# Performance work log

Measured on AMD Instinct MI355X. Metric: run time of the kernel, lower is better.

Reference implementation:

```python
import jax, jax.numpy as jnp
import numpy as np

D_MODEL, HEADS, D_FF = 768, 12, 3072
D_K = D_MODEL // HEADS
EPS = 1e-6


def _norm(x, alpha, bias):
    # NormalizationLayer: scalar alpha/bias, torch.std is unbiased (ddof=1)
    mean = jnp.mean(x, axis=-1, keepdims=True)
    std = jnp.std(x, axis=-1, ddof=1, keepdims=True)
    return alpha * (x - mean) / (std + EPS) + bias


def setup_inputs() -> dict:
    key = jax.random.key(0)
    ks = jax.random.split(key, 16)
    B, S = 2, 4096
    x = jax.random.normal(ks[0], (B, S, D_MODEL), dtype=jnp.float32)
    mask = jax.random.randint(ks[1], (B, 1, 1, S), 0, 2, dtype=jnp.int32)
    w = lambda k, o, i: (jax.random.normal(k, (o, i), dtype=jnp.float32) * 0.02)
    return {
        "x": x, "mask": mask,
        "wq": w(ks[2], D_MODEL, D_MODEL), "bq": jnp.zeros((D_MODEL,), jnp.float32),
        "wk": w(ks[3], D_MODEL, D_MODEL), "bk": jnp.zeros((D_MODEL,), jnp.float32),
        "wv": w(ks[4], D_MODEL, D_MODEL), "bv": jnp.zeros((D_MODEL,), jnp.float32),
        "wo": w(ks[5], D_MODEL, D_MODEL), "bo": jnp.zeros((D_MODEL,), jnp.float32),
        "w1": w(ks[6], D_FF, D_MODEL), "b1": jnp.zeros((D_FF,), jnp.float32),
        "w2": w(ks[7], D_MODEL, D_FF), "b2": jnp.zeros((D_MODEL,), jnp.float32),
        "alpha1": jnp.ones((1,), jnp.float32), "beta1": jnp.ones((1,), jnp.float32),
        "alpha2": jnp.ones((1,), jnp.float32), "beta2": jnp.ones((1,), jnp.float32),
    }


def reference(x, mask, wq, bq, wk, bk, wv, bv, wo, bo, w1, b1, w2, b2,
              alpha1, beta1, alpha2, beta2):
    B, S, _ = x.shape

    # --- residual connection 0: pre-norm + self-attention ---
    h = _norm(x, alpha1, beta1)
    q = (h @ wq.T + bq).reshape(B, S, HEADS, D_K).transpose(0, 2, 1, 3)  # [B,H,S,dk]
    k = (h @ wk.T + bk).reshape(B, S, HEADS, D_K).transpose(0, 2, 1, 3)
    v = (h @ wv.T + bv).reshape(B, S, HEADS, D_K).transpose(0, 2, 1, 3)
    scores = jnp.einsum('bhqd,bhkd->bhqk', q, k) / jnp.sqrt(jnp.float32(D_K))
    scores = jnp.where(mask == 0, jnp.float32(-1e9), scores)
    attn = jax.nn.softmax(scores, axis=-1)
    ctx = jnp.einsum('bhqk,bhkd->bhqd', attn, v)
    ctx = ctx.transpose(0, 2, 1, 3).reshape(B, S, D_MODEL)
    x = x + (ctx @ wo.T + bo)

    # --- residual connection 1: pre-norm + FFN ---
    h = _norm(x, alpha2, beta2)
    ff = jax.nn.relu(h @ w1.T + b1) @ w2.T + b2
    return x + ff
```

## Files before the change

kernel.cpp:

```cpp
#include <hip/hip_runtime.h>
#include <hip/hip_bf16.h>
#include <math.h>


typedef __hip_bfloat16 bf16;
typedef short short8 __attribute__((ext_vector_type(8)));
typedef short short4v __attribute__((ext_vector_type(4)));
typedef float f32x4 __attribute__((ext_vector_type(4)));

#define MFMA(A, B, C) __builtin_amdgcn_mfma_f32_16x16x32_bf16(A, B, C, 0, 0, 0)

#if __has_builtin(__builtin_amdgcn_exp2f)
#define EXP2(x) __builtin_amdgcn_exp2f(x)
#else
#define EXP2(x) exp2f(x)
#endif

#define PSWAP32(a, b) asm("v_permlane32_swap_b32 %0, %1" : "+v"(a), "+v"(b))
#define PSWAP16(a, b) asm("v_permlane16_swap_b32 %0, %1" : "+v"(a), "+v"(b))

__device__ __forceinline__ unsigned cvt_pk(float lo, float hi) {
  unsigned r;
  asm("v_cvt_pk_bf16_f32 %0, %1, %2" : "=v"(r) : "v"(lo), "v"(hi));
  return r;
}

__device__ __forceinline__ void gl_lds16(const void* g, void* l) {
  __builtin_amdgcn_global_load_lds(
      (__attribute__((address_space(1))) void*)g,
      (__attribute__((address_space(3))) void*)l, 16, 0, 0);
}

__device__ __forceinline__ short f2b(float f) {
  bf16 h = __float2bfloat16(f);
  return *reinterpret_cast<short*>(&h);
}

__global__ __launch_bounds__(256)
void prep_all(const float* __restrict__ wq, const float* __restrict__ wk,
              const float* __restrict__ wv, const float* __restrict__ wo,
              const float* __restrict__ w1, const float* __restrict__ w2,
              const float* __restrict__ bq, const float* __restrict__ bk,
              const float* __restrict__ bv, const int* __restrict__ mask,
              bf16* __restrict__ wqkvb, bf16* __restrict__ wob,
              bf16* __restrict__ w1b, bf16* __restrict__ w2b,
              float* __restrict__ bqkv,
              int* __restrict__ pos_g, int* __restrict__ nch_g,
              bf16* __restrict__ kc, bf16* __restrict__ vtc)
{
  const int t = threadIdx.x;
  if (blockIdx.x < 2) {
    const int b = blockIdx.x;
    const int* mb = mask + b * 4096;
    __shared__ int lsum[256];
    int loc = 0;
    int mv[16];
#pragma unroll
    for (int j = 0; j < 16; j++) { mv[j] = mb[t * 16 + j] ? 1 : 0; loc += mv[j]; }
    lsum[t] = loc;
    __syncthreads();
    for (int off = 1; off < 256; off <<= 1) {
      int v = (t >= off) ? lsum[t - off] : 0;
      __syncthreads();
      lsum[t] += v;
      __syncthreads();
    }
    const int nvalid = lsum[255];
    int base = lsum[t] - loc;
#pragma unroll
    for (int j = 0; j < 16; j++) {
      pos_g[b * 4096 + t * 16 + j] = mv[j] ? base : -1;
      if (mv[j]) base++;
    }
    const int npad = (nvalid + 63) & ~63;
    if (t == 0) { nch_g[b * 2] = npad >> 6; nch_g[b * 2 + 1] = npad - nvalid; }
    const int npv = npad - nvalid;
    if (npv > 0) {
      const int krows = 12 * npv;
      const short8 z = {};
      for (int task = t; task < krows * 8; task += 256) {
        const int rr = task >> 3, cc = task & 7;
        const int hh = rr / npv, r = nvalid + rr % npv;
        *(short8*)&kc[(((long)(b * 12 + hh) * 4096) + r) * 64 + cc * 8] = z;
      }
      const int vrows = 12 * 64;
      for (int task = t; task < vrows * npv; task += 256) {
        const int row = task / npv, j = nvalid + task % npv;
        const int hh = row >> 6, d = row & 63;
        vtc[((long)((b * 12 + hh) * 64 + d)) * 4096 + j] = __float2bfloat16(0.f);
      }
    }
    return;
  }
  const int i = (blockIdx.x - 2) * 256 + t;
  const int W = 147456;
  const int F = 589824;
  const float* src; bf16* dst; int off;
  if (i < W)          { src = wq; dst = wqkvb;           off = i; }
  else if (i < 2*W)   { src = wk; dst = wqkvb + 589824;  off = i - W; }
  else if (i < 3*W)   { src = wv; dst = wqkvb + 1179648; off = i - 2*W; }
  else if (i < 4*W)   { src = wo; dst = wob;             off = i - 3*W; }
  else if (i < 4*W+F) { src = w1; dst = w1b;             off = i - 4*W; }
  else                { src = w2; dst = w2b;             off = i - 4*W - F; }
  float4 v = ((const float4*)src)[off];
  short4v o;
  o.x = f2b(v.x); o.y = f2b(v.y); o.z = f2b(v.z); o.w = f2b(v.w);
  ((short4v*)dst)[off] = o;
  if (i < 2304)
    bqkv[i] = (i < 768) ? bq[i] : (i < 1536 ? bk[i - 768] : bv[i - 1536]);
}

template<typename INT>
__global__ __launch_bounds__(256)
void ln_kernel(const INT* __restrict__ x, bf16* __restrict__ out,
               const float* __restrict__ alpha, const float* __restrict__ beta)
{
  const int row = blockIdx.x;
  const long base = (long)row * 768;
  const int t = threadIdx.x;
  float v[3]; float s = 0.f, ss = 0.f;
#pragma unroll
  for (int i = 0; i < 3; i++) {
    v[i] = (float)x[base + t + i * 256];
    s += v[i]; ss += v[i] * v[i];
  }
#pragma unroll
  for (int off = 32; off > 0; off >>= 1) {
    s  += __shfl_down(s, off);
    ss += __shfl_down(ss, off);
  }
  __shared__ float red[8];
  __shared__ float stats[2];
  const int w = t >> 6;
  if ((t & 63) == 0) { red[w] = s; red[4 + w] = ss; }
  __syncthreads();
  if (t == 0) {
    float S  = red[0] + red[1] + red[2] + red[3];
    float SS = red[4] + red[5] + red[6] + red[7];
    float mean = S * (1.f / 768.f);
    float var = fmaxf((SS - 768.f * mean * mean) * (1.f / 767.f), 0.f);
    stats[0] = mean;
    stats[1] = 1.f / (sqrtf(var) + 1e-6f);
  }
  __syncthreads();
  const float mean = stats[0], rinv = stats[1];
  const float a = alpha[0], b = beta[0];
#pragma unroll
  for (int i = 0; i < 3; i++)
    out[base + t + i * 256] = __float2bfloat16(a * (v[i] - mean) * rinv + b);
}

template<int MODE, int TM, typename RT, typename OUTT>
__global__ __launch_bounds__(256)
void gemm_bt(const bf16* __restrict__ A, const bf16* __restrict__ W,
             const float* __restrict__ bias, const RT* __restrict__ R,
             OUTT* __restrict__ Cout, int M, int N, int K)
{
  constexpr int MI = TM / 32;
  __shared__ __align__(16) bf16 sA[TM * 32];
  __shared__ __align__(16) bf16 sB[128 * 32];
  const int t = threadIdx.x;
  const int w = t >> 6, lane = t & 63;
  const int lr = lane & 15, quad = lane >> 4;
  const int tm = blockIdx.x * TM, tn = blockIdx.y * 128;
  const int wm = (w >> 1) * (MI * 16), wn = (w & 1) * 64;

  const int srow = w * 16 + (lane >> 2);
  const int scol = (lane & 3) * 8;
  const bf16* Ap = A + (long)(tm + srow) * K + scol;
  const bf16* Wp = W + (long)(tn + srow) * K + scol;
  bf16* sAp = &sA[srow * 32 + scol];
  bf16* sBp = &sB[srow * 32 + scol];
  const long half = (long)64 * K;

  f32x4 acc[MI][4] = {};

  for (int kb = 0; kb < K; kb += 32) {
    gl_lds16(Ap + kb, sAp);
    if (TM == 128) gl_lds16(Ap + kb + half, sAp + 64 * 32);
    gl_lds16(Wp + kb, sBp);
    gl_lds16(Wp + kb + half, sBp + 64 * 32);
    __syncthreads();
    short8 af[MI], bfr[4];
#pragma unroll
    for (int i = 0; i < MI; i++)
      af[i] = *(const short8*)&sA[(wm + i * 16 + lr) * 32 + quad * 8];
#pragma unroll
    for (int j = 0; j < 4; j++)
      bfr[j] = *(const short8*)&sB[(wn + j * 16 + lr) * 32 + quad * 8];
#pragma unroll
    for (int i = 0; i < MI; i++)
#pragma unroll
      for (int j = 0; j < 4; j++)
        acc[i][j] = MFMA(af[i], bfr[j], acc[i][j]);
    __syncthreads();
  }

#pragma unroll
  for (int i = 0; i < MI; i++) {
#pragma unroll
    for (int j = 0; j < 4; j++) {
      const int col = tn + wn + j * 16 + lr;
      const float bv = bias[col];
#pragma unroll
      for (int r = 0; r < 4; r++) {
        const int m = tm + wm + i * 16 + quad * 4 + r;
        float vv = acc[i][j][r] + bv;
        if (MODE == 1) vv = fmaxf(vv, 0.f);
        if (MODE == 4) vv += (float)R[(long)m * N + col];
        Cout[(long)m * N + col] = (OUTT)vv;
      }
    }
  }
}

__global__ __launch_bounds__(256)
void gemm_qkv(const bf16* __restrict__ A, const bf16* __restrict__ W,
              const float* __restrict__ bias, const int* __restrict__ pos_g,
              bf16* __restrict__ Qo, bf16* __restrict__ Kc, bf16* __restrict__ Vtc)
{
  const int K = 768;
  __shared__ __align__(16) bf16 sA[128 * 32];
  __shared__ __align__(16) bf16 sB[128 * 32];
  const int t = threadIdx.x;
  const int w = t >> 6, lane = t & 63;
  const int lr = lane & 15, quad = lane >> 4;
  const int tm = blockIdx.x * 128, tn = blockIdx.y * 128;
  const int wm = (w >> 1) * 64, wn = (w & 1) * 64;

  const int srow = w * 16 + (lane >> 2);
  const int scol = (lane & 3) * 8;
  const bf16* Ap = A + (long)(tm + srow) * K + scol;
  const bf16* Wp = W + (long)(tn + srow) * K + scol;
  bf16* sAp = &sA[srow * 32 + scol];
  bf16* sBp = &sB[srow * 32 + scol];
  const long half = (long)64 * K;

  f32x4 acc[4][4] = {};

  for (int kb = 0; kb < K; kb += 32) {
    gl_lds16(Ap + kb, sAp);
    gl_lds16(Ap + kb + half, sAp + 64 * 32);
    gl_lds16(Wp + kb, sBp);
    gl_lds16(Wp + kb + half, sBp + 64 * 32);
    __syncthreads();
    short8 af[4], bfr[4];
#pragma unroll
    for (int i = 0; i < 4; i++)
      af[i] = *(const short8*)&sA[(wm + i * 16 + lr) * 32 + quad * 8];
#pragma unroll
    for (int j = 0; j < 4; j++)
      bfr[j] = *(const short8*)&sB[(wn + j * 16 + lr) * 32 + quad * 8];
#pragma unroll
    for (int i = 0; i < 4; i++)
#pragma unroll
      for (int j = 0; j < 4; j++)
        acc[i][j] = MFMA(af[i], bfr[j], acc[i][j]);
    __syncthreads();
  }

  const int region = (tn >= 1536) ? 2 : (tn >= 768 ? 1 : 0);
#pragma unroll
  for (int i = 0; i < 4; i++) {
#pragma unroll
    for (int j = 0; j < 4; j++) {
      const int col = tn + wn + j * 16 + lr;
      const int c768 = col - region * 768;
      const int hh = c768 >> 6, d = c768 & 63;
      const float bv = bias[col];
#pragma unroll
      for (int r = 0; r < 4; r++) {
        const int m = tm + wm + i * 16 + quad * 4 + r;
        const int bb = m >> 12, sdx = m & 4095;
        float vv = acc[i][j][r] + bv;
        if (region == 0) {
          vv *= 0.18033688011112042f;
          Qo[((long)(bb * 12 + hh) * 4096 + sdx) * 64 + d] = __float2bfloat16(vv);
        } else {
          const int p_ = pos_g[bb * 4096 + sdx];
          if (p_ >= 0) {
            if (region == 1)
              Kc[((long)(bb * 12 + hh) * 4096 + p_) * 64 + d] = __float2bfloat16(vv);
            else
              Vtc[((long)(bb * 12 + hh) * 64 + d) * 4096 + p_] = __float2bfloat16(vv);
          }
        }
      }
    }
  }
}

__global__ __launch_bounds__(256)
void attn_kernel(const bf16* __restrict__ Q, const bf16* __restrict__ Kg,
                 const bf16* __restrict__ Vt,
                 const int* __restrict__ nch_g, bf16* __restrict__ ctx)
{
  __shared__ __align__(16) bf16 sK[2][64 * 64];
  __shared__ __align__(16) bf16 sV[2][64 * 64];

  const int t = threadIdx.x, w = t >> 6, lane = t & 63;
  const int lr = lane & 15, quad = lane >> 4;
  const int bh = blockIdx.y, b = bh / 12, hh = bh % 12;
  const int qb = blockIdx.x * 128 + w * 32;
  const long bh_s = (long)bh * 4096;
  const int nch = nch_g[b * 2];
  const int npv = nch_g[b * 2 + 1];

  short8 qf[2][2];
#pragma unroll
  for (int qt = 0; qt < 2; qt++) {
    const bf16* qp = Q + (bh_s + qb + qt * 16 + lr) * 64 + quad * 8;
    qf[qt][0] = *(const short8*)qp;
    qf[qt][1] = *(const short8*)(qp + 32);
  }

  const int rA = w * 16 + (lane >> 3), rB = rA + 8;
  const int c8 = lane & 7;
  const bf16* kA = Kg + (bh_s + rA) * 64 + ((c8 ^ (rA & 7)) << 3);
  const bf16* kB = Kg + (bh_s + rB) * 64 + ((c8 ^ (rB & 7)) << 3);
  const bf16* vA = Vt + ((long)bh * 64 + rA) * 4096 + ((c8 ^ (rA & 7)) << 3);
  const bf16* vB = Vt + ((long)bh * 64 + rB) * 4096 + ((c8 ^ (rB & 7)) << 3);
  const int ldsA = (w * 16) * 64 + lane * 8;
  const int ldsB = ldsA + 8 * 64;

  const int cA = (quad * 8) ^ ((lr & 7) << 3);

  float l_part[2] = {};
  f32x4 Ot[4][2] = {};

  auto stage = [&](int kc, int buf) {
    gl_lds16(kA + (long)kc * 64, &sK[buf][ldsA]);
    gl_lds16(kB + (long)kc * 64, &sK[buf][ldsB]);
    gl_lds16(vA + kc, &sV[buf][ldsA]);
    gl_lds16(vB + kc, &sV[buf][ldsB]);
  };

  auto compute = [&](int buf) {
    const bf16* Kb = sK[buf];
    const bf16* Vb = sV[buf];
    f32x4 st[4][2] = {};
    __builtin_amdgcn_s_setprio(1);
#pragma unroll
    for (int kt = 0; kt < 4; kt++) {
      const int rowb = (kt * 16 + lr) * 64;
      short8 kfa = *(const short8*)&Kb[rowb + cA];
      short8 kfb = *(const short8*)&Kb[rowb + (cA ^ 32)];
      st[kt][0] = MFMA(kfa, qf[0][0], st[kt][0]);
      st[kt][0] = MFMA(kfb, qf[0][1], st[kt][0]);
      st[kt][1] = MFMA(kfa, qf[1][0], st[kt][1]);
      st[kt][1] = MFMA(kfb, qf[1][1], st[kt][1]);
    }
    __builtin_amdgcn_s_setprio(0);

    short8 pf[2][2];
#pragma unroll
    for (int qt = 0; qt < 2; qt++) {
      float p[4][4];
      float lp = 0.f;
#pragma unroll
      for (int kt = 0; kt < 4; kt++) {
#pragma unroll
        for (int r = 0; r < 4; r++) {
          p[kt][r] = EXP2(st[kt][qt][r]);
          lp += p[kt][r];
        }
      }
      l_part[qt] += lp;
      unsigned u00 = cvt_pk(p[0][0], p[0][1]), u01 = cvt_pk(p[0][2], p[0][3]);
      unsigned u10 = cvt_pk(p[1][0], p[1][1]), u11 = cvt_pk(p[1][2], p[1][3]);
      unsigned u20 = cvt_pk(p[2][0], p[2][1]), u21 = cvt_pk(p[2][2], p[2][3]);
      unsigned u30 = cvt_pk(p[3][0], p[3][1]), u31 = cvt_pk(p[3][2], p[3][3]);
      PSWAP32(u00, u10); PSWAP32(u01, u11);
      PSWAP32(u20, u30); PSWAP32(u21, u31);
      PSWAP16(u00, u10); PSWAP16(u01, u11);
      PSWAP16(u20, u30); PSWAP16(u21, u31);
      union { unsigned u[4]; short8 s8; } fa, fb;
      fa.u[0] = u00; fa.u[1] = u01; fa.u[2] = u10; fa.u[3] = u11;
      fb.u[0] = u20; fb.u[1] = u21; fb.u[2] = u30; fb.u[3] = u31;
      pf[qt][0] = fa.s8;
      pf[qt][1] = fb.s8;
    }

    __builtin_amdgcn_s_setprio(1);
#pragma unroll
    for (int dt = 0; dt < 4; dt++) {
      const int rowb = (dt * 16 + lr) * 64;
      short8 vfa = *(const short8*)&Vb[rowb + cA];
      short8 vfb = *(const short8*)&Vb[rowb + (cA ^ 32)];
      Ot[dt][0] = MFMA(vfa, pf[0][0], Ot[dt][0]);
      Ot[dt][0] = MFMA(vfb, pf[0][1], Ot[dt][0]);
      Ot[dt][1] = MFMA(vfa, pf[1][0], Ot[dt][1]);
      Ot[dt][1] = MFMA(vfb, pf[1][1], Ot[dt][1]);
    }
    __builtin_amdgcn_s_setprio(0);
  };

  stage(0, 0);
  for (int ci = 0; ci < nch; ci++) {
    __syncthreads();
    if (ci + 1 < nch) stage((ci + 1) * 64, (ci + 1) & 1);
    compute(ci & 1);
  }

#pragma unroll
  for (int qt = 0; qt < 2; qt++) {
    float l = l_part[qt];
    l += __shfl_xor(l, 16);
    l += __shfl_xor(l, 32);
    l -= (float)npv;
    const float il = (l > 0.f) ? 1.f / l : 0.f;
    const int q = qb + qt * 16 + lr;
    bf16* cp = ctx + ((long)(b * 4096 + q)) * 768 + hh * 64 + quad * 4;
#pragma unroll
    for (int dt = 0; dt < 4; dt++) {
      short4v ov;
      ov.x = f2b(Ot[dt][qt][0] * il);
      ov.y = f2b(Ot[dt][qt][1] * il);
      ov.z = f2b(Ot[dt][qt][2] * il);
      ov.w = f2b(Ot[dt][qt][3] * il);
      *(short4v*)(cp + dt * 16) = ov;
    }
  }
}

extern "C" void kernel_launch(void* const* d_in, const int* in_sizes, int n_in,
                              void* d_out, int out_size, void* d_ws, size_t ws_size,
                              hipStream_t stream)
{
  (void)in_sizes; (void)n_in; (void)out_size; (void)ws_size;
  const float* x    = (const float*)d_in[0];
  const int*   mask = (const int*)  d_in[1];
  const float* wq = (const float*)d_in[2];  const float* bq = (const float*)d_in[3];
  const float* wk = (const float*)d_in[4];  const float* bk = (const float*)d_in[5];
  const float* wv = (const float*)d_in[6];  const float* bv = (const float*)d_in[7];
  const float* wo = (const float*)d_in[8];  const float* bo = (const float*)d_in[9];
  const float* w1 = (const float*)d_in[10]; const float* b1 = (const float*)d_in[11];
  const float* w2 = (const float*)d_in[12]; const float* b2 = (const float*)d_in[13];
  const float* alpha1 = (const float*)d_in[14]; const float* beta1 = (const float*)d_in[15];
  const float* alpha2 = (const float*)d_in[16]; const float* beta2 = (const float*)d_in[17];
  float* out = (float*)d_out;

  const long WSZ = (long)768 * 768 * 2;
  const long W1SZ = (long)3072 * 768 * 2;
  const long SZB = (long)8192 * 768 * 2;
  char* ws = (char*)d_ws;
  bf16* wqkvb = (bf16*)(ws);
  bf16* wob = (bf16*)(ws + 3 * WSZ);
  bf16* w1b = (bf16*)(ws + 4 * WSZ);
  bf16* w2b = (bf16*)(ws + 4 * WSZ + W1SZ);
  char* aux = ws + 4 * WSZ + 2 * W1SZ;
  float* bqkv   = (float*)(aux);
  int*   pos_g  = (int*)(aux + 16384);
  int*   nch_g  = (int*)(aux + 81920);
  const long BASE = 16l << 20;
  bf16* h   = (bf16*)(ws + BASE);
  bf16* qws = (bf16*)(ws + BASE + 1 * SZB);
  bf16* kcw = (bf16*)(ws + BASE + 2 * SZB);
  bf16* vtc = (bf16*)(ws + BASE + 3 * SZB);
  bf16* ctx = (bf16*)(ws + BASE + 4 * SZB);
  bf16* x1  = (bf16*)(ws + BASE + 5 * SZB);
  bf16* ff  = qws;

  dim3 blk(256);

  hipLaunchKernelGGL(prep_all, dim3(6914), blk, 0, stream,
                     wq, wk, wv, wo, w1, w2, bq, bk, bv, mask,
                     wqkvb, wob, w1b, w2b, bqkv, pos_g, nch_g, kcw, vtc);

  hipLaunchKernelGGL((ln_kernel<float>), dim3(8192), blk, 0, stream, x, h, alpha1, beta1);
  hipLaunchKernelGGL(gemm_qkv, dim3(64, 18), blk, 0, stream, h, wqkvb, bqkv, pos_g, qws, kcw, vtc);
  hipLaunchKernelGGL(attn_kernel, dim3(32, 24), blk, 0, stream, qws, kcw, vtc, nch_g, ctx);
  hipLaunchKernelGGL((gemm_bt<4, 64, float, bf16>), dim3(128, 6), blk, 0, stream, ctx, wob, bo, x, x1, 8192, 768, 768);
  hipLaunchKernelGGL((ln_kernel<bf16>), dim3(8192), blk, 0, stream, x1, h, alpha2, beta2);
  hipLaunchKernelGGL((gemm_bt<1, 128, float, bf16>), dim3(64, 24), blk, 0, stream, h, w1b, b1, (const float*)nullptr, ff, 8192, 3072, 768);
  hipLaunchKernelGGL((gemm_bt<4, 64, bf16, float>), dim3(128, 6), blk, 0, stream, ff, w2b, b2, x1, out, 8192, 768, 3072);
}
```

Before: 405.8 us.

## Halve attention query tile per wave and compute row sums via MFMA with ones

Each wave now handles 16 query rows instead of 32, doubling the attention grid to 64x24 blocks, so more blocks are available to fill the GPU. The softmax denominator is now accumulated with an extra MFMA against a vector of bf16 ones rather than per-lane scalar adds followed by cross-lane shuffles. This lowers per-wave register pressure and VALU work, but each K/V tile staged in shared memory is reused by half as many queries, doubling global K/V traffic. Summing the bf16-rounded probabilities slightly changes the denominator numerics.

```diff
diff --git a/kernel.cpp b/kernel.cpp
--- a/kernel.cpp
+++ b/kernel.cpp
@@ -301,18 +301,21 @@
   const int t = threadIdx.x, w = t >> 6, lane = t & 63;
   const int lr = lane & 15, quad = lane >> 4;
   const int bh = blockIdx.y, b = bh / 12, hh = bh % 12;
-  const int qb = blockIdx.x * 128 + w * 32;
+  const int qb = blockIdx.x * 64 + w * 16;
   const long bh_s = (long)bh * 4096;
   const int nch = nch_g[b * 2];
   const int npv = nch_g[b * 2 + 1];
 
-  short8 qf[2][2];
-#pragma unroll
-  for (int qt = 0; qt < 2; qt++) {
-    const bf16* qp = Q + (bh_s + qb + qt * 16 + lr) * 64 + quad * 8;
-    qf[qt][0] = *(const short8*)qp;
-    qf[qt][1] = *(const short8*)(qp + 32);
-  }
+  short8 qf[2];
+  {
+    const bf16* qp = Q + (bh_s + qb + lr) * 64 + quad * 8;
+    qf[0] = *(const short8*)qp;
+    qf[1] = *(const short8*)(qp + 32);
+  }
+
+  short8 ones;
+#pragma unroll
+  for (int i = 0; i < 8; i++) ones[i] = (short)0x3F80;
 
   const int rA = w * 16 + (lane >> 3), rB = rA + 8;
   const int c8 = lane & 7;
@@ -325,8 +328,8 @@
 
   const int cA = (quad * 8) ^ ((lr & 7) << 3);
 
-  float l_part[2] = {};
-  f32x4 Ot[4][2] = {};
+  f32x4 lacc = {};
+  f32x4 Ot[4] = {};
 
   auto stage = [&](int kc, int buf) {
     gl_lds16(kA + (long)kc * 64, &sK[buf][ldsA]);
@@ -338,48 +341,37 @@
   auto compute = [&](int buf) {
     const bf16* Kb = sK[buf];
     const bf16* Vb = sV[buf];
-    f32x4 st[4][2] = {};
+    f32x4 st[4] = {};
     __builtin_amdgcn_s_setprio(1);
 #pragma unroll
     for (int kt = 0; kt < 4; kt++) {
       const int rowb = (kt * 16 + lr) * 64;
       short8 kfa = *(const short8*)&Kb[rowb + cA];
       short8 kfb = *(const short8*)&Kb[rowb + (cA ^ 32)];
-      st[kt][0] = MFMA(kfa, qf[0][0], st[kt][0]);
-      st[kt][0] = MFMA(kfb, qf[0][1], st[kt][0]);
-      st[kt][1] = MFMA(kfa, qf[1][0], st[kt][1]);
-      st[kt][1] = MFMA(kfb, qf[1][1], st[kt][1]);
+      st[kt] = MFMA(kfa, qf[0], st[kt]);
+      st[kt] = MFMA(kfb, qf[1], st[kt]);
     }
     __builtin_amdgcn_s_setprio(0);
 
-    short8 pf[2][2];
-#pragma unroll
-    for (int qt = 0; qt < 2; qt++) {
-      float p[4][4];
-      float lp = 0.f;
-#pragma unroll
-      for (int kt = 0; kt < 4; kt++) {
-#pragma unroll
-        for (int r = 0; r < 4; r++) {
-          p[kt][r] = EXP2(st[kt][qt][r]);
-          lp += p[kt][r];
-        }
-      }
-      l_part[qt] += lp;
-      unsigned u00 = cvt_pk(p[0][0], p[0][1]), u01 = cvt_pk(p[0][2], p[0][3]);
-      unsigned u10 = cvt_pk(p[1][0], p[1][1]), u11 = cvt_pk(p[1][2], p[1][3]);
-      unsigned u20 = cvt_pk(p[2][0], p[2][1]), u21 = cvt_pk(p[2][2], p[2][3]);
-      unsigned u30 = cvt_pk(p[3][0], p[3][1]), u31 = cvt_pk(p[3][2], p[3][3]);
-      PSWAP32(u00, u10); PSWAP32(u01, u11);
-      PSWAP32(u20, u30); PSWAP32(u21, u31);
-      PSWAP16(u00, u10); PSWAP16(u01, u11);
-      PSWAP16(u20, u30); PSWAP16(u21, u31);
-      union { unsigned u[4]; short8 s8; } fa, fb;
-      fa.u[0] = u00; fa.u[1] = u01; fa.u[2] = u10; fa.u[3] = u11;
-      fb.u[0] = u20; fb.u[1] = u21; fb.u[2] = u30; fb.u[3] = u31;
-      pf[qt][0] = fa.s8;
-      pf[qt][1] = fb.s8;
-    }
+    float p[4][4];
+#pragma unroll
+    for (int kt = 0; kt < 4; kt++)
+#pragma unroll
+      for (int r = 0; r < 4; r++)
+        p[kt][r] = EXP2(st[kt][r]);
+
+    unsigned u00 = cvt_pk(p[0][0], p[0][1]), u01 = cvt_pk(p[0][2], p[0][3]);
+    unsigned u10 = cvt_pk(p[1][0], p[1][1]), u11 = cvt_pk(p[1][2], p[1][3]);
+    unsigned u20 = cvt_pk(p[2][0], p[2][1]), u21 = cvt_pk(p[2][2], p[2][3]);
+    unsigned u30 = cvt_pk(p[3][0], p[3][1]), u31 = cvt_pk(p[3][2], p[3][3]);
+    PSWAP32(u00, u10); PSWAP32(u01, u11);
+    PSWAP32(u20, u30); PSWAP32(u21, u31);
+    PSWAP16(u00, u10); PSWAP16(u01, u11);
+    PSWAP16(u20, u30); PSWAP16(u21, u31);
+    union { unsigned u[4]; short8 s8; } fa, fb;
+    fa.u[0] = u00; fa.u[1] = u01; fa.u[2] = u10; fa.u[3] = u11;
+    fb.u[0] = u20; fb.u[1] = u21; fb.u[2] = u30; fb.u[3] = u31;
+    const short8 pf0 = fa.s8, pf1 = fb.s8;
 
     __builtin_amdgcn_s_setprio(1);
 #pragma unroll
@@ -387,11 +379,11 @@
       const int rowb = (dt * 16 + lr) * 64;
       short8 vfa = *(const short8*)&Vb[rowb + cA];
       short8 vfb = *(const short8*)&Vb[rowb + (cA ^ 32)];
-      Ot[dt][0] = MFMA(vfa, pf[0][0], Ot[dt][0]);
-      Ot[dt][0] = MFMA(vfb, pf[0][1], Ot[dt][0]);
-      Ot[dt][1] = MFMA(vfa, pf[1][0], Ot[dt][1]);
-      Ot[dt][1] = MFMA(vfb, pf[1][1], Ot[dt][1]);
-    }
+      Ot[dt] = MFMA(vfa, pf0, Ot[dt]);
+      Ot[dt] = MFMA(vfb, pf1, Ot[dt]);
+    }
+    lacc = MFMA(ones, pf0, lacc);
+    lacc = MFMA(ones, pf1, lacc);
     __builtin_amdgcn_s_setprio(0);
   };
 
@@ -402,22 +394,18 @@
     compute(ci & 1);
   }
 
-#pragma unroll
-  for (int qt = 0; qt < 2; qt++) {
-    float l = l_part[qt];
-    l += __shfl_xor(l, 16);
-    l += __shfl_xor(l, 32);
-    l -= (float)npv;
+  {
+    const float l = lacc[0] - (float)npv;
     const float il = (l > 0.f) ? 1.f / l : 0.f;
-    const int q = qb + qt * 16 + lr;
+    const int q = qb + lr;
     bf16* cp = ctx + ((long)(b * 4096 + q)) * 768 + hh * 64 + quad * 4;
 #pragma unroll
     for (int dt = 0; dt < 4; dt++) {
       short4v ov;
-      ov.x = f2b(Ot[dt][qt][0] * il);
-      ov.y = f2b(Ot[dt][qt][1] * il);
-      ov.z = f2b(Ot[dt][qt][2] * il);
-      ov.w = f2b(Ot[dt][qt][3] * il);
+      ov.x = f2b(Ot[dt][0] * il);
+      ov.y = f2b(Ot[dt][1] * il);
+      ov.z = f2b(Ot[dt][2] * il);
+      ov.w = f2b(Ot[dt][3] * il);
       *(short4v*)(cp + dt * 16) = ov;
     }
   }
@@ -469,7 +457,7 @@
 
   hipLaunchKernelGGL((ln_kernel<float>), dim3(8192), blk, 0, stream, x, h, alpha1, beta1);
   hipLaunchKernelGGL(gemm_qkv, dim3(64, 18), blk, 0, stream, h, wqkvb, bqkv, pos_g, qws, kcw, vtc);
-  hipLaunchKernelGGL(attn_kernel, dim3(32, 24), blk, 0, stream, qws, kcw, vtc, nch_g, ctx);
+  hipLaunchKernelGGL(attn_kernel, dim3(64, 24), blk, 0, stream, qws, kcw, vtc, nch_g, ctx);
   hipLaunchKernelGGL((gemm_bt<4, 64, float, bf16>), dim3(128, 6), blk, 0, stream, ctx, wob, bo, x, x1, 8192, 768, 768);
   hipLaunchKernelGGL((ln_kernel<bf16>), dim3(8192), blk, 0, stream, x1, h, alpha2, beta2);
   hipLaunchKernelGGL((gemm_bt<1, 128, float, bf16>), dim3(64, 24), blk, 0, stream, h, w1b, b1, (const float*)nullptr, ff, 8192, 3072, 768);
```

Result: no change. 411.6 us (+1.4%).

## Double-buffer GEMM LDS tiles and compute softmax row sums via MFMA

Applied to the files above, without the earlier changes.

Both GEMM kernels now use double-buffered shared-memory tiles: the next K-slice is issued before computing on the current one, which removes the second barrier per iteration and overlaps global-to-LDS loads with MFMA work. In attention, the softmax denominator is no longer a VALU sum plus cross-lane shuffles. It comes from an extra MFMA against a vector of bf16 ones, using the already-rounded bf16 probabilities. This doubles LDS use in the GEMMs, which may lower occupancy, and adds four MFMAs per chunk in attention. The row sum now matches the bf16-rounded values fed to PV.

```diff
diff --git a/kernel.cpp b/kernel.cpp
--- a/kernel.cpp
+++ b/kernel.cpp
@@ -157,8 +157,8 @@
              OUTT* __restrict__ Cout, int M, int N, int K)
 {
   constexpr int MI = TM / 32;
-  __shared__ __align__(16) bf16 sA[TM * 32];
-  __shared__ __align__(16) bf16 sB[128 * 32];
+  __shared__ __align__(16) bf16 sA[2][TM * 32];
+  __shared__ __align__(16) bf16 sB[2][128 * 32];
   const int t = threadIdx.x;
   const int w = t >> 6, lane = t & 63;
   const int lr = lane & 15, quad = lane >> 4;
@@ -167,33 +167,39 @@
 
   const int srow = w * 16 + (lane >> 2);
   const int scol = (lane & 3) * 8;
+  const int soff = srow * 32 + scol;
   const bf16* Ap = A + (long)(tm + srow) * K + scol;
   const bf16* Wp = W + (long)(tn + srow) * K + scol;
-  bf16* sAp = &sA[srow * 32 + scol];
-  bf16* sBp = &sB[srow * 32 + scol];
   const long half = (long)64 * K;
 
+  auto stage = [&](int kb, int bi) {
+    gl_lds16(Ap + kb, &sA[bi][soff]);
+    if (TM == 128) gl_lds16(Ap + kb + half, &sA[bi][soff + 64 * 32]);
+    gl_lds16(Wp + kb, &sB[bi][soff]);
+    gl_lds16(Wp + kb + half, &sB[bi][soff + 64 * 32]);
+  };
+
   f32x4 acc[MI][4] = {};
 
-  for (int kb = 0; kb < K; kb += 32) {
-    gl_lds16(Ap + kb, sAp);
-    if (TM == 128) gl_lds16(Ap + kb + half, sAp + 64 * 32);
-    gl_lds16(Wp + kb, sBp);
-    gl_lds16(Wp + kb + half, sBp + 64 * 32);
+  stage(0, 0);
+  int bi = 0;
+  for (int kb = 0; kb < K; kb += 32, bi ^= 1) {
     __syncthreads();
+    if (kb + 32 < K) stage(kb + 32, bi ^ 1);
+    const bf16* sAb = sA[bi];
+    const bf16* sBb = sB[bi];
     short8 af[MI], bfr[4];
 #pragma unroll
     for (int i = 0; i < MI; i++)
-      af[i] = *(const short8*)&sA[(wm + i * 16 + lr) * 32 + quad * 8];
+      af[i] = *(const short8*)&sAb[(wm + i * 16 + lr) * 32 + quad * 8];
 #pragma unroll
     for (int j = 0; j < 4; j++)
-      bfr[j] = *(const short8*)&sB[(wn + j * 16 + lr) * 32 + quad * 8];
+      bfr[j] = *(const short8*)&sBb[(wn + j * 16 + lr) * 32 + quad * 8];
 #pragma unroll
     for (int i = 0; i < MI; i++)
 #pragma unroll
       for (int j = 0; j < 4; j++)
         acc[i][j] = MFMA(af[i], bfr[j], acc[i][j]);
-    __syncthreads();
   }
 
 #pragma unroll
@@ -220,8 +226,8 @@
               bf16* __restrict__ Qo, bf16* __restrict__ Kc, bf16* __restrict__ Vtc)
 {
   const int K = 768;
-  __shared__ __align__(16) bf16 sA[128 * 32];
-  __shared__ __align__(16) bf16 sB[128 * 32];
+  __shared__ __align__(16) bf16 sA[2][128 * 32];
+  __shared__ __align__(16) bf16 sB[2][128 * 32];
   const int t = threadIdx.x;
   const int w = t >> 6, lane = t & 63;
   const int lr = lane & 15, quad = lane >> 4;
@@ -230,33 +236,39 @@
 
   const int srow = w * 16 + (lane >> 2);
   const int scol = (lane & 3) * 8;
+  const int soff = srow * 32 + scol;
   const bf16* Ap = A + (long)(tm + srow) * K + scol;
   const bf16* Wp = W + (long)(tn + srow) * K + scol;
-  bf16* sAp = &sA[srow * 32 + scol];
-  bf16* sBp = &sB[srow * 32 + scol];
   const long half = (long)64 * K;
 
+  auto stage = [&](int kb, int bi) {
+    gl_lds16(Ap + kb, &sA[bi][soff]);
+    gl_lds16(Ap + kb + half, &sA[bi][soff + 64 * 32]);
+    gl_lds16(Wp + kb, &sB[bi][soff]);
+    gl_lds16(Wp + kb + half, &sB[bi][soff + 64 * 32]);
+  };
+
   f32x4 acc[4][4] = {};
 
-  for (int kb = 0; kb < K; kb += 32) {
-    gl_lds16(Ap + kb, sAp);
-    gl_lds16(Ap + kb + half, sAp + 64 * 32);
-    gl_lds16(Wp + kb, sBp);
-    gl_lds16(Wp + kb + half, sBp + 64 * 32);
+  stage(0, 0);
+  int bi = 0;
+  for (int kb = 0; kb < K; kb += 32, bi ^= 1) {
     __syncthreads();
+    if (kb + 32 < K) stage(kb + 32, bi ^ 1);
+    const bf16* sAb = sA[bi];
+    const bf16* sBb = sB[bi];
     short8 af[4], bfr[4];
 #pragma unroll
     for (int i = 0; i < 4; i++)
-      af[i] = *(const short8*)&sA[(wm + i * 16 + lr) * 32 + quad * 8];
+      af[i] = *(const short8*)&sAb[(wm + i * 16 + lr) * 32 + quad * 8];
 #pragma unroll
     for (int j = 0; j < 4; j++)
-      bfr[j] = *(const short8*)&sB[(wn + j * 16 + lr) * 32 + quad * 8];
+      bfr[j] = *(const short8*)&sBb[(wn + j * 16 + lr) * 32 + quad * 8];
 #pragma unroll
     for (int i = 0; i < 4; i++)
 #pragma unroll
       for (int j = 0; j < 4; j++)
         acc[i][j] = MFMA(af[i], bfr[j], acc[i][j]);
-    __syncthreads();
   }
 
   const int region = (tn >= 1536) ? 2 : (tn >= 768 ? 1 : 0);
@@ -314,6 +326,10 @@
     qf[qt][1] = *(const short8*)(qp + 32);
   }
 
+  short8 ones;
+#pragma unroll
+  for (int i = 0; i < 8; i++) ones[i] = (short)0x3F80;
+
   const int rA = w * 16 + (lane >> 3), rB = rA + 8;
   const int c8 = lane & 7;
   const bf16* kA = Kg + (bh_s + rA) * 64 + ((c8 ^ (rA & 7)) << 3);
@@ -325,7 +341,7 @@
 
   const int cA = (quad * 8) ^ ((lr & 7) << 3);
 
-  float l_part[2] = {};
+  f32x4 lacc[2] = {};
   f32x4 Ot[4][2] = {};
 
   auto stage = [&](int kc, int buf) {
@@ -356,16 +372,11 @@
 #pragma unroll
     for (int qt = 0; qt < 2; qt++) {
       float p[4][4];
-      float lp = 0.f;
-#pragma unroll
-      for (int kt = 0; kt < 4; kt++) {
-#pragma unroll
-        for (int r = 0; r < 4; r++) {
+#pragma unroll
+      for (int kt = 0; kt < 4; kt++)
+#pragma unroll
+        for (int r = 0; r < 4; r++)
           p[kt][r] = EXP2(st[kt][qt][r]);
-          lp += p[kt][r];
-        }
-      }
-      l_part[qt] += lp;
       unsigned u00 = cvt_pk(p[0][0], p[0][1]), u01 = cvt_pk(p[0][2], p[0][3]);
       unsigned u10 = cvt_pk(p[1][0], p[1][1]), u11 = cvt_pk(p[1][2], p[1][3]);
       unsigned u20 = cvt_pk(p[2][0], p[2][1]), u21 = cvt_pk(p[2][2], p[2][3]);
@@ -392,6 +403,10 @@
       Ot[dt][1] = MFMA(vfa, pf[1][0], Ot[dt][1]);
       Ot[dt][1] = MFMA(vfb, pf[1][1], Ot[dt][1]);
     }
+    lacc[0] = MFMA(ones, pf[0][0], lacc[0]);
+    lacc[0] = MFMA(ones, pf[0][1], lacc[0]);
+    lacc[1] = MFMA(ones, pf[1][0], lacc[1]);
+    lacc[1] = MFMA(ones, pf[1][1], lacc[1]);
     __builtin_amdgcn_s_setprio(0);
   };
 
@@ -404,10 +419,7 @@
 
 #pragma unroll
   for (int qt = 0; qt < 2; qt++) {
-    float l = l_part[qt];
-    l += __shfl_xor(l, 16);
-    l += __shfl_xor(l, 32);
-    l -= (float)npv;
+    const float l = lacc[qt][0] - (float)npv;
     const float il = (l > 0.f) ? 1.f / l : 0.f;
     const int q = qb + qt * 16 + lr;
     bf16* cp = ctx + ((long)(b * 4096 + q)) * 768 + hh * 64 + quad * 4;
```

Result: no change. 398.0 us (-1.9%).
